# Kernel tuning notes

Hardware: AMD Instinct MI355X
Metric: run time of the kernel (lower is better)

The kernel has to match this reference:

```python
import jax, jax.numpy as jnp
import numpy as np

# Config matching init_kwargs
C = 256
NUM_HEADS = 8
WIN = (6, 6, 6)
B, D, H, W = 2, 48, 48, 48
LN_EPS = 1e-5


def setup_inputs() -> dict:
    key = jax.random.key(0)
    ks = jax.random.split(key, 4)
    shp = (B, C, D, H, W)
    return {
        "q_map": jax.random.normal(ks[0], shp, jnp.float32),
        "k_map": jax.random.normal(ks[1], shp, jnp.float32),
        "v_map": jax.random.normal(ks[2], shp, jnp.float32),
        "ln_q_w": jnp.ones((C,), jnp.float32),
        "ln_q_b": jnp.zeros((C,), jnp.float32),
        "ln_kv_w": jnp.ones((C,), jnp.float32),
        "ln_kv_b": jnp.zeros((C,), jnp.float32),
        "proj_w": jax.random.normal(ks[3], (C, C), jnp.float32) * 0.02,  # torch Linear weight [out, in]
        "proj_b": jnp.zeros((C,), jnp.float32),
    }


def _layernorm(x, w, b):
    mu = jnp.mean(x, axis=-1, keepdims=True)
    var = jnp.mean(jnp.square(x - mu), axis=-1, keepdims=True)
    return (x - mu) * jax.lax.rsqrt(var + LN_EPS) * w + b


def _window_partition(x):  # x: [B, C, D, H, W] -> [B*nw, wd*wh*ww, C]
    wd, wh, ww = WIN
    x = jnp.transpose(x, (0, 2, 3, 4, 1))  # [B, D, H, W, C]
    b, d, h, w, c = x.shape
    # D,H,W chosen divisible by window; pad amounts are zero (kept general via exact reshape)
    x = x.reshape(b, d // wd, wd, h // wh, wh, w // ww, ww, c)
    x = jnp.transpose(x, (0, 1, 3, 5, 2, 4, 6, 7))
    return x.reshape(-1, wd * wh * ww, c)


def _window_reverse(windows, b, d, h, w):  # -> [B, C, D, H, W]
    wd, wh, ww = WIN
    c = windows.shape[-1]
    x = windows.reshape(b, d // wd, h // wh, w // ww, wd, wh, ww, c)
    x = jnp.transpose(x, (0, 1, 4, 2, 5, 3, 6, 7)).reshape(b, d, h, w, c)
    return jnp.transpose(x, (0, 4, 1, 2, 3))


def reference(q_map, k_map, v_map, ln_q_w, ln_q_b, ln_kv_w, ln_kv_b, proj_w, proj_b):
    b, c, d, h, w = q_map.shape
    nh = NUM_HEADS
    dh = c // nh

    q = _layernorm(_window_partition(q_map), ln_q_w, ln_q_b)   # [Bw, N, C]
    k = _layernorm(_window_partition(k_map), ln_kv_w, ln_kv_b)
    v = _layernorm(_window_partition(v_map), ln_kv_w, ln_kv_b)

    bw, n, _ = q.shape
    q = q.reshape(bw, n, nh, dh)
    k = k.reshape(bw, n, nh, dh)
    v = v.reshape(bw, n, nh, dh)

    scale = 1.0 / np.sqrt(dh).astype(np.float32)
    scores = jnp.einsum('bqhd,bkhd->bhqk', q, k) * scale      # [Bw, H, N, N]
    attn = jax.nn.softmax(scores, axis=-1)
    out = jnp.einsum('bhqk,bkhd->bqhd', attn, v).reshape(bw, n, c)

    out = out @ proj_w.T + proj_b                              # nn.Linear: x W^T + b
    return _window_reverse(out, b, d, h, w)
```

## Files before the change

### kernel.cpp

```cpp
#include <hip/hip_runtime.h>

#define C_    256
#define DHW   110592
#define NTOK  221184
#define NSEQ  216
#define NH    8
#define DH    32

typedef _Float16 half8  __attribute__((ext_vector_type(8)));
typedef _Float16 half4v __attribute__((ext_vector_type(4)));
typedef __fp16   fp16x2 __attribute__((ext_vector_type(2)));
typedef float    float4v  __attribute__((ext_vector_type(4)));
typedef float    float16v __attribute__((ext_vector_type(16)));

union H8U4 { half8 h; uint4 u; };
union H2U1 { fp16x2 h; unsigned u; };

static __device__ __forceinline__ unsigned pkrtz(float a, float b) {
    H2U1 t; t.h = __builtin_amdgcn_cvt_pkrtz(a, b); return t.u;
}

__global__ __launch_bounds__(256) void k_convert_w(const float* __restrict__ w,
                                                   _Float16* __restrict__ wh) {
    int i = blockIdx.x * 256 + threadIdx.x;
#pragma unroll
    for (int j = 0; j < 4; ++j) {
        int idx = i + j * 16384;
        wh[idx] = (_Float16)w[idx];
    }
}

__global__ __launch_bounds__(256) void k_ln(
    const float* __restrict__ q_map, const float* __restrict__ k_map,
    const float* __restrict__ v_map,
    const float* __restrict__ lnq_w, const float* __restrict__ lnq_b,
    const float* __restrict__ lnkv_w, const float* __restrict__ lnkv_b,
    _Float16* __restrict__ qo, _Float16* __restrict__ ko, _Float16* __restrict__ vo)
{
    __shared__ float ps1[8][32];
    __shared__ float ps2[8][32];
    const int tid = threadIdx.x;
    const int g = tid >> 5, t = tid & 31;
    const int m = blockIdx.y;
    const float* xm = (m == 0) ? q_map : (m == 1) ? k_map : v_map;
    _Float16*   xo = (m == 0) ? qo    : (m == 1) ? ko    : vo;
    const float* wv = (m == 0) ? lnq_w : lnkv_w;
    const float* bv = (m == 0) ? lnq_b : lnkv_b;
    const float sc = (m == 0) ? (0.17677669529663687f * 1.4426950408889634f) : 1.0f;

    const int blk = blockIdx.x;
    const int b = blk / 3456;
    const int pos = (blk - b * 3456) * 32 + t;

    const int d = pos / 2304, rem = pos % 2304, h = rem / 48, w = rem % 48;
    const int wi = (d / 6) * 64 + (h / 6) * 8 + (w / 6);
    const int n = (d % 6) * 36 + (h % 6) * 6 + (w % 6);
    const long outRow = (long)(b * 512 + wi) * NSEQ + n;

    const float* xp = xm + (size_t)b * C_ * DHW + pos;
    float x[32];
    float s1 = 0.f, s2 = 0.f;
#pragma unroll
    for (int i = 0; i < 32; ++i) {
        x[i] = xp[(size_t)(g * 32 + i) * DHW];
        s1 += x[i]; s2 += x[i] * x[i];
    }
    ps1[g][t] = s1; ps2[g][t] = s2;
    __syncthreads();
    float a1 = 0.f, a2 = 0.f;
#pragma unroll
    for (int gg = 0; gg < 8; ++gg) { a1 += ps1[gg][t]; a2 += ps2[gg][t]; }
    float mu = a1 * (1.f / 256.f);
    float rstd = rsqrtf(a2 * (1.f / 256.f) - mu * mu + 1e-5f);

    _Float16* op = xo + (size_t)outRow * C_ + g * 32;
#pragma unroll
    for (int i0 = 0; i0 < 32; i0 += 8) {
        half8 y;
#pragma unroll
        for (int i = 0; i < 8; ++i) {
            int c = g * 32 + i0 + i;
            y[i] = (_Float16)(((x[i0 + i] - mu) * rstd * wv[c] + bv[c]) * sc);
        }
        *(half8*)(op + i0) = y;
    }
}

__global__ __launch_bounds__(448) void k_attn(
    const _Float16* __restrict__ qh, const _Float16* __restrict__ kh,
    const _Float16* __restrict__ vh, _Float16* __restrict__ ao)
{
    __shared__ _Float16 Ks[224 * 32];
    __shared__ _Float16 Vb[28 * 256];
    __shared__ float rsum[7 * 32];

    const int tid = threadIdx.x;
    const int wave = tid >> 6, lane = tid & 63;
    const int l31 = lane & 31, h = lane >> 5;
    const int win = blockIdx.x >> 3, head = blockIdx.x & 7;
    const size_t base = ((size_t)win * NSEQ) * C_ + head * DH;

#pragma unroll
    for (int it = 0; it < 2; ++it) {
        int idx = tid + it * 448;
        int r = idx >> 2, c8 = idx & 3;
        half8 kv{};
        if (r < NSEQ) kv = *(const half8*)(kh + base + (size_t)r * C_ + c8 * 8);
        *(half8*)(&Ks[r * 32 + ((c8 ^ ((r >> 1) & 3)) * 8)]) = kv;
    }
#pragma unroll
    for (int it = 0; it < 2; ++it) {
        int idx = tid + it * 448;
        int kb = idx >> 5, d = idx & 31;
        const _Float16* vp = vh + base + (size_t)(kb * 8) * C_ + d;
        half8 vv{};
#pragma unroll
        for (int j = 0; j < 8; ++j) {
            int r = kb * 8 + j;
            vv[j] = (r < NSEQ) ? vp[(size_t)j * C_] : (_Float16)0;
        }
        *(half8*)(&Vb[kb * 256 + d * 8]) = vv;
    }

    const int qrow = wave * 32 + l31;
    half8 qf0{}, qf1{};
    if (qrow < NSEQ) {
        const _Float16* qp = qh + base + (size_t)qrow * C_ + h * 8;
        qf0 = *(const half8*)(qp);
        qf1 = *(const half8*)(qp + 16);
    }
    __syncthreads();

    float16v O{};
    float sum = 0.f;

#pragma unroll
    for (int kt = 0; kt < 7; ++kt) {
        const int krow = kt * 32 + l31;
        const int sw = (krow >> 1) & 3;
        half8 kf0 = *(const half8*)(&Ks[krow * 32 + ((h ^ sw) * 8)]);
        half8 kf1 = *(const half8*)(&Ks[krow * 32 + (((2 + h) ^ sw) * 8)]);
        float16v s{};
        s = __builtin_amdgcn_mfma_f32_32x32x16_f16(kf0, qf0, s, 0, 0, 0);
        s = __builtin_amdgcn_mfma_f32_32x32x16_f16(kf1, qf1, s, 0, 0, 0);

        const int RV = (kt == 6) ? 12 : 16;
        float p[16];
#pragma unroll
        for (int r = 0; r < 16; ++r) p[r] = (r < RV) ? exp2f(s[r]) : 0.f;
#pragma unroll
        for (int r = 0; r < 16; ++r) sum += p[r];

#pragma unroll
        for (int m = 0; m < 2; ++m) {
            const int rb = m * 8;
            unsigned a0 = pkrtz(p[rb + 0], p[rb + 1]);
            unsigned a1 = pkrtz(p[rb + 2], p[rb + 3]);
            unsigned a2 = pkrtz(p[rb + 4], p[rb + 5]);
            unsigned a3 = pkrtz(p[rb + 6], p[rb + 7]);
            asm volatile("v_permlane32_swap_b32 %0, %1" : "+v"(a0), "+v"(a2));
            asm volatile("v_permlane32_swap_b32 %0, %1" : "+v"(a1), "+v"(a3));
            H8U4 pa;
            pa.u.x = a0; pa.u.y = a1; pa.u.z = a2; pa.u.w = a3;
            half8 vb = *(const half8*)(&Vb[(kt * 4 + m * 2 + h) * 256 + l31 * 8]);
            O = __builtin_amdgcn_mfma_f32_32x32x16_f16(pa.h, vb, O, 0, 0, 0);
        }
    }

    float tot = sum + __shfl_xor(sum, 32);
    if (h == 0) rsum[wave * 32 + l31] = 1.f / tot;
    __syncthreads();

    float4 r0 = *(const float4*)(&rsum[wave * 32 + 4 * h + 0]);
    float4 r1 = *(const float4*)(&rsum[wave * 32 + 4 * h + 8]);
    float4 r2 = *(const float4*)(&rsum[wave * 32 + 4 * h + 16]);
    float4 r3 = *(const float4*)(&rsum[wave * 32 + 4 * h + 24]);
    float rv[16] = {r0.x, r0.y, r0.z, r0.w, r1.x, r1.y, r1.z, r1.w,
                    r2.x, r2.y, r2.z, r2.w, r3.x, r3.y, r3.z, r3.w};

    _Float16* aop = ao + ((size_t)win * NSEQ + wave * 32) * C_ + head * DH + l31;
#pragma unroll
    for (int r = 0; r < 16; ++r) {
        int qp = (r & 3) + 8 * (r >> 2) + 4 * h;
        if (wave * 32 + qp < NSEQ)
            aop[(size_t)qp * C_] = (_Float16)(O[r] * rv[r]);
    }
}

__global__ __launch_bounds__(256) void k_proj(
    const _Float16* __restrict__ ah, const _Float16* __restrict__ wh,
    const float* __restrict__ pb, float* __restrict__ out)
{
    __shared__ _Float16 As[64 * 264];
    const int tid = threadIdx.x;
    const int wave = tid >> 6, lane = tid & 63;
    const int l15 = lane & 15, g = lane >> 4;
    const long tok0 = (long)blockIdx.x * 64;

    {
        int r = tid >> 2, c8 = tid & 3;
        long tok = tok0 + r;
        int b = (int)(tok / DHW);
        int pos = (int)(tok - (long)b * DHW);
        int d = pos / 2304, rem = pos % 2304, hh = rem / 48, ww = rem % 48;
        int wi = (d / 6) * 64 + (hh / 6) * 8 + (ww / 6);
        int n = (d % 6) * 36 + (hh % 6) * 6 + (ww % 6);
        const _Float16* src = ah + ((size_t)(b * 512 + wi) * NSEQ + n) * C_;
        _Float16* dst = &As[r * 264];
#pragma unroll
        for (int i = 0; i < 8; ++i)
            *(half8*)(dst + c8 * 8 + i * 32) = *(const half8*)(src + c8 * 8 + i * 32);
    }
    __syncthreads();

    const int b0 = (int)(tok0 / DHW);
    const int pos0 = (int)(tok0 - (long)b0 * DHW);
    float* ob = out + (size_t)b0 * C_ * DHW + pos0;

#pragma unroll
    for (int ct = 0; ct < 4; ++ct) {
        const int c0 = wave * 64 + ct * 16;
        half8 afr[8];
#pragma unroll
        for (int kc = 0; kc < 8; ++kc)
            afr[kc] = *(const half8*)(wh + (size_t)(c0 + l15) * C_ + kc * 32 + g * 8);
        float4 bq = *(const float4*)(pb + c0 + g * 4);
#pragma unroll
        for (int tt = 0; tt < 4; ++tt) {
            float4v o = {bq.x, bq.y, bq.z, bq.w};
#pragma unroll
            for (int kc = 0; kc < 8; ++kc) {
                half8 bfr = *(const half8*)(&As[(tt * 16 + l15) * 264 + kc * 32 + g * 8]);
                o = __builtin_amdgcn_mfma_f32_16x16x32_f16(afr[kc], bfr, o, 0, 0, 0);
            }
#pragma unroll
            for (int r = 0; r < 4; ++r)
                ob[(size_t)(c0 + g * 4 + r) * DHW + tt * 16 + l15] = o[r];
        }
    }
}

extern "C" void kernel_launch(void* const* d_in, const int* in_sizes, int n_in,
                              void* d_out, int out_size, void* d_ws, size_t ws_size,
                              hipStream_t stream)
{
    const float* q_map  = (const float*)d_in[0];
    const float* k_map  = (const float*)d_in[1];
    const float* v_map  = (const float*)d_in[2];
    const float* lnq_w  = (const float*)d_in[3];
    const float* lnq_b  = (const float*)d_in[4];
    const float* lnkv_w = (const float*)d_in[5];
    const float* lnkv_b = (const float*)d_in[6];
    const float* proj_w = (const float*)d_in[7];
    const float* proj_b = (const float*)d_in[8];
    float* out = (float*)d_out;

    const size_t SZ = (size_t)NTOK * C_;
    _Float16* qh = (_Float16*)d_ws;
    _Float16* kh = qh + SZ;
    _Float16* vh = kh + SZ;
    _Float16* ah = vh + SZ;
    _Float16* wh = ah + SZ;

    k_convert_w<<<64, 256, 0, stream>>>(proj_w, wh);
    k_ln<<<dim3(6912, 3), 256, 0, stream>>>(q_map, k_map, v_map,
                                            lnq_w, lnq_b, lnkv_w, lnkv_b, qh, kh, vh);
    k_attn<<<8192, 448, 0, stream>>>(qh, kh, vh, ah);
    k_proj<<<3456, 256, 0, stream>>>(ah, wh, proj_b, out);
}
```

Baseline: 509.2 us.

## Vectorize LayerNorm loads with float4 and remap attention block-to-window order

The LayerNorm kernel now handles 64 spatial positions per block, each thread loading float4 vectors across 16 channels, and reduces the partial statistics through a padded shared-memory table. The scale factor is folded into weight and bias held in registers. This aims for wider, better-coalesced global reads and fewer blocks, at the cost of more registers and more index arithmetic per output row. Separately, the attention kernel permutes its block index so that consecutive blocks take the same head in different windows, which changes cache locality and scheduling order.

After: 457.7 us. 10.1% less time.

```diff
diff --git a/kernel.cpp b/kernel.cpp
--- a/kernel.cpp
+++ b/kernel.cpp
@@ -37,10 +37,11 @@
     const float* __restrict__ lnkv_w, const float* __restrict__ lnkv_b,
     _Float16* __restrict__ qo, _Float16* __restrict__ ko, _Float16* __restrict__ vo)
 {
-    __shared__ float ps1[8][32];
-    __shared__ float ps2[8][32];
+    __shared__ float ps1[64][20];
+    __shared__ float ps2[64][20];
     const int tid = threadIdx.x;
-    const int g = tid >> 5, t = tid & 31;
+    const int tx = tid & 15;
+    const int cg = tid >> 4;
     const int m = blockIdx.y;
     const float* xm = (m == 0) ? q_map : (m == 1) ? k_map : v_map;
     _Float16*   xo = (m == 0) ? qo    : (m == 1) ? ko    : vo;
@@ -48,41 +49,69 @@
     const float* bv = (m == 0) ? lnq_b : lnkv_b;
     const float sc = (m == 0) ? (0.17677669529663687f * 1.4426950408889634f) : 1.0f;
 
-    const int blk = blockIdx.x;
-    const int b = blk / 3456;
-    const int pos = (blk - b * 3456) * 32 + t;
-
-    const int d = pos / 2304, rem = pos % 2304, h = rem / 48, w = rem % 48;
-    const int wi = (d / 6) * 64 + (h / 6) * 8 + (w / 6);
-    const int n = (d % 6) * 36 + (h % 6) * 6 + (w % 6);
-    const long outRow = (long)(b * 512 + wi) * NSEQ + n;
-
-    const float* xp = xm + (size_t)b * C_ * DHW + pos;
-    float x[32];
-    float s1 = 0.f, s2 = 0.f;
-#pragma unroll
-    for (int i = 0; i < 32; ++i) {
-        x[i] = xp[(size_t)(g * 32 + i) * DHW];
-        s1 += x[i]; s2 += x[i] * x[i];
-    }
-    ps1[g][t] = s1; ps2[g][t] = s2;
+    const long pg = (long)blockIdx.x * 64;
+    const int b = (int)(pg / DHW);
+    const int pos = (int)(pg - (long)b * DHW);
+
+    const float* xp = xm + (size_t)b * C_ * DHW + pos + tx * 4;
+    float4 x[16];
+    float s1[4] = {0.f, 0.f, 0.f, 0.f};
+    float s2[4] = {0.f, 0.f, 0.f, 0.f};
+#pragma unroll
+    for (int i = 0; i < 16; ++i) {
+        x[i] = *(const float4*)(xp + (size_t)(cg * 16 + i) * DHW);
+        s1[0] += x[i].x; s2[0] += x[i].x * x[i].x;
+        s1[1] += x[i].y; s2[1] += x[i].y * x[i].y;
+        s1[2] += x[i].z; s2[2] += x[i].z * x[i].z;
+        s1[3] += x[i].w; s2[3] += x[i].w * x[i].w;
+    }
+#pragma unroll
+    for (int j = 0; j < 4; ++j) { ps1[tx * 4 + j][cg] = s1[j]; ps2[tx * 4 + j][cg] = s2[j]; }
     __syncthreads();
-    float a1 = 0.f, a2 = 0.f;
-#pragma unroll
-    for (int gg = 0; gg < 8; ++gg) { a1 += ps1[gg][t]; a2 += ps2[gg][t]; }
-    float mu = a1 * (1.f / 256.f);
-    float rstd = rsqrtf(a2 * (1.f / 256.f) - mu * mu + 1e-5f);
-
-    _Float16* op = xo + (size_t)outRow * C_ + g * 32;
-#pragma unroll
-    for (int i0 = 0; i0 < 32; i0 += 8) {
-        half8 y;
+
+    float mu[4], rs[4];
+#pragma unroll
+    for (int j = 0; j < 4; ++j) {
+        float a1 = 0.f, a2 = 0.f;
+#pragma unroll
+        for (int cc = 0; cc < 4; ++cc) {
+            float4 p1 = *(const float4*)(&ps1[tx * 4 + j][cc * 4]);
+            float4 p2 = *(const float4*)(&ps2[tx * 4 + j][cc * 4]);
+            a1 += (p1.x + p1.y) + (p1.z + p1.w);
+            a2 += (p2.x + p2.y) + (p2.z + p2.w);
+        }
+        mu[j] = a1 * (1.f / 256.f);
+        rs[j] = rsqrtf(a2 * (1.f / 256.f) - mu[j] * mu[j] + 1e-5f);
+    }
+
+    float wr[16], br[16];
+#pragma unroll
+    for (int cc = 0; cc < 4; ++cc) {
+        float4 wq = *(const float4*)(wv + cg * 16 + cc * 4);
+        float4 bq = *(const float4*)(bv + cg * 16 + cc * 4);
+        wr[cc * 4 + 0] = wq.x * sc; br[cc * 4 + 0] = bq.x * sc;
+        wr[cc * 4 + 1] = wq.y * sc; br[cc * 4 + 1] = bq.y * sc;
+        wr[cc * 4 + 2] = wq.z * sc; br[cc * 4 + 2] = bq.z * sc;
+        wr[cc * 4 + 3] = wq.w * sc; br[cc * 4 + 3] = bq.w * sc;
+    }
+
+#pragma unroll
+    for (int j = 0; j < 4; ++j) {
+        const int p = pos + tx * 4 + j;
+        const int d = p / 2304, rem = p % 2304, hh = rem / 48, ww = rem % 48;
+        const int wi = (d / 6) * 64 + (hh / 6) * 8 + (ww / 6);
+        const int n = (d % 6) * 36 + (hh % 6) * 6 + (ww % 6);
+        _Float16* op = xo + ((size_t)(b * 512 + wi) * NSEQ + n) * C_ + cg * 16;
+        half8 y0, y1;
 #pragma unroll
         for (int i = 0; i < 8; ++i) {
-            int c = g * 32 + i0 + i;
-            y[i] = (_Float16)(((x[i0 + i] - mu) * rstd * wv[c] + bv[c]) * sc);
-        }
-        *(half8*)(op + i0) = y;
+            float xa = (j == 0) ? x[i].x : (j == 1) ? x[i].y : (j == 2) ? x[i].z : x[i].w;
+            float xb = (j == 0) ? x[i + 8].x : (j == 1) ? x[i + 8].y : (j == 2) ? x[i + 8].z : x[i + 8].w;
+            y0[i] = (_Float16)((xa - mu[j]) * rs[j] * wr[i] + br[i]);
+            y1[i] = (_Float16)((xb - mu[j]) * rs[j] * wr[i + 8] + br[i + 8]);
+        }
+        *(half8*)op = y0;
+        *(half8*)(op + 8) = y1;
     }
 }
 
@@ -97,7 +126,8 @@
     const int tid = threadIdx.x;
     const int wave = tid >> 6, lane = tid & 63;
     const int l31 = lane & 31, h = lane >> 5;
-    const int win = blockIdx.x >> 3, head = blockIdx.x & 7;
+    const int o = ((blockIdx.x & 7) << 10) | (blockIdx.x >> 3);
+    const int win = o >> 3, head = o & 7;
     const size_t base = ((size_t)win * NSEQ) * C_ + head * DH;
 
 #pragma unroll
@@ -263,7 +293,7 @@
     _Float16* wh = ah + SZ;
 
     k_convert_w<<<64, 256, 0, stream>>>(proj_w, wh);
-    k_ln<<<dim3(6912, 3), 256, 0, stream>>>(q_map, k_map, v_map,
+    k_ln<<<dim3(3456, 3), 256, 0, stream>>>(q_map, k_map, v_map,
                                             lnq_w, lnq_b, lnkv_w, lnkv_b, qh, kh, vh);
     k_attn<<<8192, 448, 0, stream>>>(qh, kh, vh, ah);
     k_proj<<<3456, 256, 0, stream>>>(ah, wh, proj_b, out);
```
